# Optimization experiments

Measured on AMD Instinct MI355X. Metric: run time of the kernel, lower is better.

## Reference

```python
import jax, jax.numpy as jnp
import numpy as np

N_NODES = 200000
D_FEAT = 512
B = 512
S1, S2 = 25, 10  # num_samples for layer 0 and layer 1
HID = 256
NUM_CLASSES = 50


def setup_inputs() -> dict:
    key = jax.random.key(0)
    ks = jax.random.split(key, 10)
    sc = 0.05
    return {
        "features": jax.random.normal(ks[0], (N_NODES, D_FEAT), jnp.float32),
        "W_self0": jax.random.normal(ks[1], (D_FEAT, HID), jnp.float32) * sc,
        "W_neigh0": jax.random.normal(ks[2], (D_FEAT, HID), jnp.float32) * sc,
        "W_self1": jax.random.normal(ks[3], (2 * HID, HID), jnp.float32) * sc,
        "W_neigh1": jax.random.normal(ks[4], (2 * HID, HID), jnp.float32) * sc,
        "W_pred": jax.random.normal(ks[5], (2 * HID, NUM_CLASSES), jnp.float32) * sc,
        "b_pred": jnp.zeros((NUM_CLASSES,), jnp.float32),
        "samples0": jax.random.randint(ks[6], (B,), 0, N_NODES, jnp.int64 if jax.config.read('jax_enable_x64') else jnp.int32),
        "samples1": jax.random.randint(ks[7], (B * S2,), 0, N_NODES, jnp.int64 if jax.config.read('jax_enable_x64') else jnp.int32),
        "samples2": jax.random.randint(ks[8], (B * S2 * S1,), 0, N_NODES, jnp.int64 if jax.config.read('jax_enable_x64') else jnp.int32),
    }


def _mean_agg(h_self, h_neigh, W_self, W_neigh, act):
    # h_self: [n, d_in]; h_neigh: [n, S, d_in]
    neigh_mean = h_neigh.mean(axis=1)
    out = jnp.concatenate([h_self @ W_self, neigh_mean @ W_neigh], axis=-1)
    return act(out)


def reference(features, W_self0, W_neigh0, W_self1, W_neigh1, W_pred, b_pred,
              samples0, samples1, samples2):
    # irregular gathers of the support tree
    h0 = features[samples0]                      # [B, d]
    h1 = features[samples1]                      # [B*S2, d]
    h2 = features[samples2]                      # [B*S2*S1, d]
    # layer 0 (relu, dim_mult=1): applied at hops 0 and 1
    n0 = _mean_agg(h0, h1.reshape(B, S2, D_FEAT), W_self0, W_neigh0, jax.nn.relu)          # [B, 2H]
    n1 = _mean_agg(h1, h2.reshape(B * S2, S1, D_FEAT), W_self0, W_neigh0, jax.nn.relu)     # [B*S2, 2H]
    # layer 1 (identity act, dim_mult=2)
    out = _mean_agg(n0, n1.reshape(B, S2, 2 * HID), W_self1, W_neigh1, lambda x: x)        # [B, 2H]
    # F.normalize(p=2, dim=1), eps=1e-12
    norm = out / jnp.maximum(jnp.linalg.norm(out, axis=1, keepdims=True), 1e-12)
    logits = norm @ W_pred + b_pred
    return logits
```

## Files before the change

kernel.cpp:

```cpp
#include <hip/hip_runtime.h>

#define DF   512
#define HID2 512
#define NHID 256
#define NCLS 50
#define NB   512

typedef __attribute__((ext_vector_type(8))) short short8;
typedef __attribute__((ext_vector_type(4))) float float4v;

__device__ __forceinline__ float b2f(unsigned short u) {
    union { unsigned int i; float f; } v; v.i = ((unsigned int)u) << 16; return v.f;
}
__device__ __forceinline__ unsigned short f2b(float f) {
    union { float f; unsigned int u; } v; v.f = f;
    unsigned int r = v.u + 0x7FFFu + ((v.u >> 16) & 1u);
    return (unsigned short)(r >> 16);
}

__global__ void prep_weights(const float* __restrict__ W0, const float* __restrict__ W1,
                             const float* __restrict__ W2, const float* __restrict__ W3,
                             unsigned short* __restrict__ Wt) {
    __shared__ unsigned short T[64][66];
    const float* W = (blockIdx.z == 0) ? W0 : (blockIdx.z == 1) ? W1 :
                     (blockIdx.z == 2) ? W2 : W3;
    unsigned short* Out = Wt + (size_t)blockIdx.z * NHID * DF;
    const int k0 = blockIdx.x * 64, n0 = blockIdx.y * 64;
    const int t = threadIdx.x;
#pragma unroll
    for (int p = 0; p < 4; ++p) {
        const int k = p * 16 + (t >> 4);
        const int n = (t & 15) * 4;
        const float4 v = *(const float4*)(W + (size_t)(k0 + k) * NHID + n0 + n);
        T[n + 0][k] = f2b(v.x);
        T[n + 1][k] = f2b(v.y);
        T[n + 2][k] = f2b(v.z);
        T[n + 3][k] = f2b(v.w);
    }
    __syncthreads();
#pragma unroll
    for (int p = 0; p < 4; ++p) {
        const int n = p * 16 + (t >> 4);
        const int k = (t & 15) * 4;
        ushort4 o;
        o.x = T[n][k]; o.y = T[n][k + 1]; o.z = T[n][k + 2]; o.w = T[n][k + 3];
        *(ushort4*)(Out + (size_t)(n0 + n) * DF + k0 + k) = o;
    }
}

__global__ void gather_cvt(const float* __restrict__ feat, const int* __restrict__ idx,
                           unsigned short* __restrict__ out) {
    const int r = blockIdx.x;
    const int col = threadIdx.x * 4;
    const float4 v = *(const float4*)(feat + (size_t)idx[r] * DF + col);
    ushort4 o; o.x = f2b(v.x); o.y = f2b(v.y); o.z = f2b(v.z); o.w = f2b(v.w);
    *(ushort4*)(out + (size_t)r * DF + col) = o;
}

template <int GS>
__global__ void gather_mean(const float* __restrict__ feat, const int* __restrict__ idx,
                            unsigned short* __restrict__ out, float inv) {
    const int g = blockIdx.x;
    const int col = threadIdx.x * 4;
    float4 acc = make_float4(0.f, 0.f, 0.f, 0.f);
#pragma unroll
    for (int j = 0; j < GS; ++j) {
        const float4 v = *(const float4*)(feat + (size_t)idx[g * GS + j] * DF + col);
        acc.x += v.x; acc.y += v.y; acc.z += v.z; acc.w += v.w;
    }
    ushort4 o;
    o.x = f2b(acc.x * inv); o.y = f2b(acc.y * inv);
    o.z = f2b(acc.z * inv); o.w = f2b(acc.w * inv);
    *(ushort4*)(out + (size_t)g * DF + col) = o;
}

template <int GS>
__global__ void mean_bf16(const unsigned short* __restrict__ in,
                          unsigned short* __restrict__ out, float inv) {
    const int g = blockIdx.x;
    const int col = threadIdx.x * 4;
    float acc[4] = {0.f, 0.f, 0.f, 0.f};
#pragma unroll
    for (int j = 0; j < GS; ++j) {
        const ushort4 v = *(const ushort4*)(in + ((size_t)g * GS + j) * DF + col);
        acc[0] += b2f(v.x); acc[1] += b2f(v.y); acc[2] += b2f(v.z); acc[3] += b2f(v.w);
    }
    ushort4 o;
    o.x = f2b(acc[0] * inv); o.y = f2b(acc[1] * inv);
    o.z = f2b(acc[2] * inv); o.w = f2b(acc[3] * inv);
    *(ushort4*)(out + (size_t)g * DF + col) = o;
}

__global__ __launch_bounds__(256) void gemm_dual_mfma(
        const unsigned short* __restrict__ A1, const unsigned short* __restrict__ A2,
        const unsigned short* __restrict__ W1t, const unsigned short* __restrict__ W2t,
        void* __restrict__ Cout, int relu, int cfp32) {
    __shared__ unsigned short As[64][72];
    __shared__ unsigned short Bs[64][72];
    const int tid = threadIdx.x;
    const int wave = tid >> 6;
    const int lane = tid & 63;
    const int m0 = blockIdx.y * 64;
    const int nb = blockIdx.x * 64;
    const unsigned short* A  = (nb < 256) ? A1 : A2;
    const unsigned short* Wt = (nb < 256) ? W1t : W2t;
    const int n0 = nb & 255;

    const int sr = tid >> 3;
    const int sk = (tid & 7) * 8;

    float4v acc[4];
#pragma unroll
    for (int i = 0; i < 4; ++i) acc[i] = (float4v)(0.f);

    const int am = wave * 16 + (lane & 15);
    const int kq = (lane >> 4) * 8;

    for (int k0 = 0; k0 < DF; k0 += 64) {
        *(uint4*)&As[sr][sk]      = *(const uint4*)(A  + (size_t)(m0 + sr) * DF + k0 + sk);
        *(uint4*)&As[sr + 32][sk] = *(const uint4*)(A  + (size_t)(m0 + sr + 32) * DF + k0 + sk);
        *(uint4*)&Bs[sr][sk]      = *(const uint4*)(Wt + (size_t)(n0 + sr) * DF + k0 + sk);
        *(uint4*)&Bs[sr + 32][sk] = *(const uint4*)(Wt + (size_t)(n0 + sr + 32) * DF + k0 + sk);
        __syncthreads();
#pragma unroll
        for (int ks = 0; ks < 64; ks += 32) {
            const short8 af = *(const short8*)&As[am][ks + kq];
#pragma unroll
            for (int nt = 0; nt < 4; ++nt) {
                const short8 bf = *(const short8*)&Bs[nt * 16 + (lane & 15)][ks + kq];
                acc[nt] = __builtin_amdgcn_mfma_f32_16x16x32_bf16(af, bf, acc[nt], 0, 0, 0);
            }
        }
        __syncthreads();
    }

#pragma unroll
    for (int nt = 0; nt < 4; ++nt) {
        const int gcol = nb + nt * 16 + (lane & 15);
#pragma unroll
        for (int r = 0; r < 4; ++r) {
            const int grow = m0 + wave * 16 + (lane >> 4) * 4 + r;
            float v = acc[nt][r];
            if (relu) v = fmaxf(v, 0.f);
            if (cfp32) ((float*)Cout)[(size_t)grow * HID2 + gcol] = v;
            else ((unsigned short*)Cout)[(size_t)grow * HID2 + gcol] = f2b(v);
        }
    }
}

__global__ void normalize_pred(const float* __restrict__ outb,
                               const float* __restrict__ Wp,
                               const float* __restrict__ bp,
                               float* __restrict__ logits) {
    __shared__ float row[HID2];
    __shared__ float red[256];
    const int r = blockIdx.x;
    const int t = threadIdx.x;
    const float2 v = *(const float2*)(outb + (size_t)r * HID2 + t * 2);
    row[t * 2] = v.x;
    row[t * 2 + 1] = v.y;
    red[t] = v.x * v.x + v.y * v.y;
    __syncthreads();
    for (int s = 128; s > 0; s >>= 1) {
        if (t < s) red[t] += red[t + s];
        __syncthreads();
    }
    const float scale = 1.0f / fmaxf(sqrtf(red[0]), 1e-12f);
    if (t < NCLS) {
        float acc = 0.f;
        for (int k = 0; k < HID2; ++k) acc += row[k] * Wp[k * NCLS + t];
        logits[r * NCLS + t] = acc * scale + bp[t];
    }
}

extern "C" void kernel_launch(void* const* d_in, const int* in_sizes, int n_in,
                              void* d_out, int out_size, void* d_ws, size_t ws_size,
                              hipStream_t stream) {
    const float* feat    = (const float*)d_in[0];
    const float* Wself0  = (const float*)d_in[1];
    const float* Wneigh0 = (const float*)d_in[2];
    const float* Wself1  = (const float*)d_in[3];
    const float* Wneigh1 = (const float*)d_in[4];
    const float* Wpred   = (const float*)d_in[5];
    const float* bpred   = (const float*)d_in[6];
    const int* s0 = (const int*)d_in[7];
    const int* s1 = (const int*)d_in[8];
    const int* s2 = (const int*)d_in[9];

    unsigned short* u = (unsigned short*)d_ws;
    unsigned short* h2mean = u;
    unsigned short* h1bf   = h2mean + 5120 * 512;
    unsigned short* n1     = h1bf   + 5120 * 512;
    unsigned short* h1mean = n1     + 5120 * 512;
    unsigned short* h0bf   = h1mean + 512 * 512;
    unsigned short* n1mean = h0bf   + 512 * 512;
    unsigned short* n0     = n1mean + 512 * 512;
    unsigned short* Wt     = n0     + 512 * 512;
    float* outb = (float*)(Wt + 4 * NHID * DF);
    unsigned short* Wt_s0 = Wt;
    unsigned short* Wt_n0 = Wt + 1 * NHID * DF;
    unsigned short* Wt_s1 = Wt + 2 * NHID * DF;
    unsigned short* Wt_n1 = Wt + 3 * NHID * DF;

    prep_weights<<<dim3(8, 4, 4), 256, 0, stream>>>(Wself0, Wneigh0, Wself1, Wneigh1, Wt);
    gather_cvt<<<NB, 128, 0, stream>>>(feat, s0, h0bf);
    gather_cvt<<<NB * 10, 128, 0, stream>>>(feat, s1, h1bf);
    mean_bf16<10><<<NB, 128, 0, stream>>>(h1bf, h1mean, 0.1f);
    gather_mean<25><<<NB * 10, 128, 0, stream>>>(feat, s2, h2mean, 1.f / 25.f);

    gemm_dual_mfma<<<dim3(8, 80), 256, 0, stream>>>(h1bf, h2mean, Wt_s0, Wt_n0, n1, 1, 0);
    mean_bf16<10><<<NB, 128, 0, stream>>>(n1, n1mean, 0.1f);
    gemm_dual_mfma<<<dim3(8, 8), 256, 0, stream>>>(h0bf, h1mean, Wt_s0, Wt_n0, n0, 1, 0);
    gemm_dual_mfma<<<dim3(8, 8), 256, 0, stream>>>(n0, n1mean, Wt_s1, Wt_n1, outb, 0, 1);

    normalize_pred<<<NB, 256, 0, stream>>>(outb, Wpred, bpred, (float*)d_out);
}
```

Measured before the change: 573.8 us.

## Fuse preprocessing kernels, merge layer-0 GEMMs, split prediction reduction

Merges the weight transpose, the h0/h1 gathers, h1 mean and h2 gather-mean into one launch dispatched by block index. h1mean is now computed directly from fp32 features rather than from the bf16 copy. The two layer-0 GEMMs (hop 0 and hop 1) become one launch with 88 row-blocks. The final projection in normalize_pred is split across four thread groups over K, so 200 threads do the dot products instead of 50. The aim is to cut launch count and tail idle time and to raise parallelism in the last kernel, at the cost of more branching inside the kernels.

```diff
diff --git a/kernel.cpp b/kernel.cpp
--- a/kernel.cpp
+++ b/kernel.cpp
@@ -18,67 +18,98 @@
     return (unsigned short)(r >> 16);
 }
 
-__global__ void prep_weights(const float* __restrict__ W0, const float* __restrict__ W1,
-                             const float* __restrict__ W2, const float* __restrict__ W3,
-                             unsigned short* __restrict__ Wt) {
+__global__ __launch_bounds__(256) void preprocess(
+        const float* __restrict__ feat,
+        const float* __restrict__ W0, const float* __restrict__ W1,
+        const float* __restrict__ W2, const float* __restrict__ W3,
+        unsigned short* __restrict__ Wt,
+        const int* __restrict__ s0, const int* __restrict__ s1,
+        const int* __restrict__ s2,
+        unsigned short* __restrict__ h0bf, unsigned short* __restrict__ h1bf,
+        unsigned short* __restrict__ h1mean, unsigned short* __restrict__ h2mean) {
     __shared__ unsigned short T[64][66];
-    const float* W = (blockIdx.z == 0) ? W0 : (blockIdx.z == 1) ? W1 :
-                     (blockIdx.z == 2) ? W2 : W3;
-    unsigned short* Out = Wt + (size_t)blockIdx.z * NHID * DF;
-    const int k0 = blockIdx.x * 64, n0 = blockIdx.y * 64;
+    const int b = blockIdx.x;
     const int t = threadIdx.x;
-#pragma unroll
-    for (int p = 0; p < 4; ++p) {
-        const int k = p * 16 + (t >> 4);
-        const int n = (t & 15) * 4;
-        const float4 v = *(const float4*)(W + (size_t)(k0 + k) * NHID + n0 + n);
-        T[n + 0][k] = f2b(v.x);
-        T[n + 1][k] = f2b(v.y);
-        T[n + 2][k] = f2b(v.z);
-        T[n + 3][k] = f2b(v.w);
-    }
-    __syncthreads();
-#pragma unroll
-    for (int p = 0; p < 4; ++p) {
-        const int n = p * 16 + (t >> 4);
-        const int k = (t & 15) * 4;
+
+    if (b < 128) {
+        const int x = b & 7, y = (b >> 3) & 3, z = b >> 5;
+        const float* W = (z == 0) ? W0 : (z == 1) ? W1 : (z == 2) ? W2 : W3;
+        unsigned short* Out = Wt + (size_t)z * NHID * DF;
+        const int k0 = x * 64, n0 = y * 64;
+#pragma unroll
+        for (int p = 0; p < 4; ++p) {
+            const int k = p * 16 + (t >> 4);
+            const int n = (t & 15) * 4;
+            const float4 v = *(const float4*)(W + (size_t)(k0 + k) * NHID + n0 + n);
+            T[n + 0][k] = f2b(v.x);
+            T[n + 1][k] = f2b(v.y);
+            T[n + 2][k] = f2b(v.z);
+            T[n + 3][k] = f2b(v.w);
+        }
+        __syncthreads();
+#pragma unroll
+        for (int p = 0; p < 4; ++p) {
+            const int n = p * 16 + (t >> 4);
+            const int k = (t & 15) * 4;
+            ushort4 o;
+            o.x = T[n][k]; o.y = T[n][k + 1]; o.z = T[n][k + 2]; o.w = T[n][k + 3];
+            *(ushort4*)(Out + (size_t)(n0 + n) * DF + k0 + k) = o;
+        }
+        return;
+    }
+
+    const int sub = t >> 7;
+    const int col = (t & 127) * 4;
+
+    if (b < 384) {
+        const int r = (b - 128) * 2 + sub;
+        const float4 v = *(const float4*)(feat + (size_t)s0[r] * DF + col);
+        ushort4 o; o.x = f2b(v.x); o.y = f2b(v.y); o.z = f2b(v.z); o.w = f2b(v.w);
+        *(ushort4*)(h0bf + (size_t)r * DF + col) = o;
+        return;
+    }
+    if (b < 2944) {
+        const int r = (b - 384) * 2 + sub;
+        const float4 v = *(const float4*)(feat + (size_t)s1[r] * DF + col);
+        ushort4 o; o.x = f2b(v.x); o.y = f2b(v.y); o.z = f2b(v.z); o.w = f2b(v.w);
+        *(ushort4*)(h1bf + (size_t)r * DF + col) = o;
+        return;
+    }
+    if (b < 3200) {
+        const int g = (b - 2944) * 2 + sub;
+        float ax = 0.f, ay = 0.f, az = 0.f, aw = 0.f;
+#pragma unroll
+        for (int j = 0; j < 10; ++j) {
+            const float4 v = *(const float4*)(feat + (size_t)s1[g * 10 + j] * DF + col);
+            ax += v.x; ay += v.y; az += v.z; aw += v.w;
+        }
         ushort4 o;
-        o.x = T[n][k]; o.y = T[n][k + 1]; o.z = T[n][k + 2]; o.w = T[n][k + 3];
-        *(ushort4*)(Out + (size_t)(n0 + n) * DF + k0 + k) = o;
-    }
-}
-
-__global__ void gather_cvt(const float* __restrict__ feat, const int* __restrict__ idx,
-                           unsigned short* __restrict__ out) {
-    const int r = blockIdx.x;
-    const int col = threadIdx.x * 4;
-    const float4 v = *(const float4*)(feat + (size_t)idx[r] * DF + col);
-    ushort4 o; o.x = f2b(v.x); o.y = f2b(v.y); o.z = f2b(v.z); o.w = f2b(v.w);
-    *(ushort4*)(out + (size_t)r * DF + col) = o;
-}
-
-template <int GS>
-__global__ void gather_mean(const float* __restrict__ feat, const int* __restrict__ idx,
-                            unsigned short* __restrict__ out, float inv) {
-    const int g = blockIdx.x;
-    const int col = threadIdx.x * 4;
-    float4 acc = make_float4(0.f, 0.f, 0.f, 0.f);
-#pragma unroll
-    for (int j = 0; j < GS; ++j) {
-        const float4 v = *(const float4*)(feat + (size_t)idx[g * GS + j] * DF + col);
-        acc.x += v.x; acc.y += v.y; acc.z += v.z; acc.w += v.w;
-    }
-    ushort4 o;
-    o.x = f2b(acc.x * inv); o.y = f2b(acc.y * inv);
-    o.z = f2b(acc.z * inv); o.w = f2b(acc.w * inv);
-    *(ushort4*)(out + (size_t)g * DF + col) = o;
+        o.x = f2b(ax * 0.1f); o.y = f2b(ay * 0.1f);
+        o.z = f2b(az * 0.1f); o.w = f2b(aw * 0.1f);
+        *(ushort4*)(h1mean + (size_t)g * DF + col) = o;
+        return;
+    }
+    {
+        const int g = (b - 3200) * 2 + sub;
+        float ax = 0.f, ay = 0.f, az = 0.f, aw = 0.f;
+#pragma unroll
+        for (int j = 0; j < 25; ++j) {
+            const float4 v = *(const float4*)(feat + (size_t)s2[g * 25 + j] * DF + col);
+            ax += v.x; ay += v.y; az += v.z; aw += v.w;
+        }
+        const float inv = 1.f / 25.f;
+        ushort4 o;
+        o.x = f2b(ax * inv); o.y = f2b(ay * inv);
+        o.z = f2b(az * inv); o.w = f2b(aw * inv);
+        *(ushort4*)(h2mean + (size_t)g * DF + col) = o;
+    }
 }
 
 template <int GS>
 __global__ void mean_bf16(const unsigned short* __restrict__ in,
                           unsigned short* __restrict__ out, float inv) {
-    const int g = blockIdx.x;
-    const int col = threadIdx.x * 4;
+    const int g = blockIdx.x * 2 + (threadIdx.x >> 7);
+    const int col = (threadIdx.x & 127) * 4;
     float acc[4] = {0.f, 0.f, 0.f, 0.f};
 #pragma unroll
     for (int j = 0; j < GS; ++j) {
@@ -89,6 +120,66 @@
     o.x = f2b(acc[0] * inv); o.y = f2b(acc[1] * inv);
     o.z = f2b(acc[2] * inv); o.w = f2b(acc[3] * inv);
     *(ushort4*)(out + (size_t)g * DF + col) = o;
+}
+
+__global__ __launch_bounds__(256) void gemm_fused01(
+        const unsigned short* __restrict__ A1a, const unsigned short* __restrict__ A2a,
+        const unsigned short* __restrict__ A1b, const unsigned short* __restrict__ A2b,
+        const unsigned short* __restrict__ W1t, const unsigned short* __restrict__ W2t,
+        unsigned short* __restrict__ C1, unsigned short* __restrict__ C2) {
+    __shared__ unsigned short As[64][72];
+    __shared__ unsigned short Bs[64][72];
+    const int tid = threadIdx.x;
+    const int wave = tid >> 6;
+    const int lane = tid & 63;
+    const bool second = (blockIdx.y >= 80);
+    const int m0 = (second ? (blockIdx.y - 80) : blockIdx.y) * 64;
+    const int nb = blockIdx.x * 64;
+    const unsigned short* A1 = second ? A1b : A1a;
+    const unsigned short* A2 = second ? A2b : A2a;
+    unsigned short* C = second ? C2 : C1;
+    const unsigned short* A  = (nb < 256) ? A1 : A2;
+    const unsigned short* Wt = (nb < 256) ? W1t : W2t;
+    const int n0 = nb & 255;
+
+    const int sr = tid >> 3;
+    const int sk = (tid & 7) * 8;
+
+    float4v acc[4];
+#pragma unroll
+    for (int i = 0; i < 4; ++i) acc[i] = (float4v)(0.f);
+
+    const int am = wave * 16 + (lane & 15);
+    const int kq = (lane >> 4) * 8;
+
+    for (int k0 = 0; k0 < DF; k0 += 64) {
+        *(uint4*)&As[sr][sk]      = *(const uint4*)(A  + (size_t)(m0 + sr) * DF + k0 + sk);
+        *(uint4*)&As[sr + 32][sk] = *(const uint4*)(A  + (size_t)(m0 + sr + 32) * DF + k0 + sk);
+        *(uint4*)&Bs[sr][sk]      = *(const uint4*)(Wt + (size_t)(n0 + sr) * DF + k0 + sk);
+        *(uint4*)&Bs[sr + 32][sk] = *(const uint4*)(Wt + (size_t)(n0 + sr + 32) * DF + k0 + sk);
+        __syncthreads();
+#pragma unroll
+        for (int ks = 0; ks < 64; ks += 32) {
+            const short8 af = *(const short8*)&As[am][ks + kq];
+#pragma unroll
+            for (int nt = 0; nt < 4; ++nt) {
+                const short8 bf = *(const short8*)&Bs[nt * 16 + (lane & 15)][ks + kq];
+                acc[nt] = __builtin_amdgcn_mfma_f32_16x16x32_bf16(af, bf, acc[nt], 0, 0, 0);
+            }
+        }
+        __syncthreads();
+    }
+
+#pragma unroll
+    for (int nt = 0; nt < 4; ++nt) {
+        const int gcol = nb + nt * 16 + (lane & 15);
+#pragma unroll
+        for (int r = 0; r < 4; ++r) {
+            const int grow = m0 + wave * 16 + (lane >> 4) * 4 + r;
+            const float v = fmaxf(acc[nt][r], 0.f);
+            C[(size_t)grow * HID2 + gcol] = f2b(v);
+        }
+    }
 }
 
 __global__ __launch_bounds__(256) void gemm_dual_mfma(
@@ -148,12 +239,14 @@
     }
 }
 
-__global__ void normalize_pred(const float* __restrict__ outb,
-                               const float* __restrict__ Wp,
-                               const float* __restrict__ bp,
-                               float* __restrict__ logits) {
+__global__ __launch_bounds__(256) void normalize_pred(
+        const float* __restrict__ outb,
+        const float* __restrict__ Wp,
+        const float* __restrict__ bp,
+        float* __restrict__ logits) {
     __shared__ float row[HID2];
     __shared__ float red[256];
+    __shared__ float part[4][64];
     const int r = blockIdx.x;
     const int t = threadIdx.x;
     const float2 v = *(const float2*)(outb + (size_t)r * HID2 + t * 2);
@@ -166,10 +259,18 @@
         __syncthreads();
     }
     const float scale = 1.0f / fmaxf(sqrtf(red[0]), 1e-12f);
+    const int c = t & 63;
+    const int q = t >> 6;
+    float acc = 0.f;
+    if (c < NCLS) {
+#pragma unroll 4
+        for (int k = q * 128; k < q * 128 + 128; ++k) acc += row[k] * Wp[k * NCLS + c];
+    }
+    part[q][c] = acc;
+    __syncthreads();
     if (t < NCLS) {
-        float acc = 0.f;
-        for (int k = 0; k < HID2; ++k) acc += row[k] * Wp[k * NCLS + t];
-        logits[r * NCLS + t] = acc * scale + bp[t];
+        logits[r * NCLS + t] =
+            (part[0][t] + part[1][t] + part[2][t] + part[3][t]) * scale + bp[t];
     }
 }
 
@@ -202,16 +303,11 @@
     unsigned short* Wt_s1 = Wt + 2 * NHID * DF;
     unsigned short* Wt_n1 = Wt + 3 * NHID * DF;
 
-    prep_weights<<<dim3(8, 4, 4), 256, 0, stream>>>(Wself0, Wneigh0, Wself1, Wneigh1, Wt);
-    gather_cvt<<<NB, 128, 0, stream>>>(feat, s0, h0bf);
-    gather_cvt<<<NB * 10, 128, 0, stream>>>(feat, s1, h1bf);
-    mean_bf16<10><<<NB, 128, 0, stream>>>(h1bf, h1mean, 0.1f);
-    gather_mean<25><<<NB * 10, 128, 0, stream>>>(feat, s2, h2mean, 1.f / 25.f);
-
-    gemm_dual_mfma<<<dim3(8, 80), 256, 0, stream>>>(h1bf, h2mean, Wt_s0, Wt_n0, n1, 1, 0);
-    mean_bf16<10><<<NB, 128, 0, stream>>>(n1, n1mean, 0.1f);
-    gemm_dual_mfma<<<dim3(8, 8), 256, 0, stream>>>(h0bf, h1mean, Wt_s0, Wt_n0, n0, 1, 0);
+    preprocess<<<5760, 256, 0, stream>>>(feat, Wself0, Wneigh0, Wself1, Wneigh1, Wt,
+                                         s0, s1, s2, h0bf, h1bf, h1mean, h2mean);
+    gemm_fused01<<<dim3(8, 88), 256, 0, stream>>>(h1bf, h2mean, h0bf, h1mean,
+                                                  Wt_s0, Wt_n0, n1, n0);
+    mean_bf16<10><<<256, 256, 0, stream>>>(n1, n1mean, 0.1f);
     gemm_dual_mfma<<<dim3(8, 8), 256, 0, stream>>>(n0, n1mean, Wt_s1, Wt_n1, outb, 0, 1);
-
     normalize_pred<<<NB, 256, 0, stream>>>(outb, Wpred, bpred, (float*)d_out);
 }
```

Result: faster. 542.8 us (-5.4%).
